# Performance work log

Measured on AMD Instinct MI355X. Metric: run time of the kernel, lower is better.

## Reference

```python
import jax, jax.numpy as jnp
import numpy as np

N, M, K = 500000, 8, 16


def setup_inputs() -> dict:
    key = jax.random.key(0)
    kp, kq, ka, kx = jax.random.split(key, 4)
    p = jax.random.normal(kp, (N, M), dtype=jnp.float32)
    q = jax.random.normal(kq, (N, M), dtype=jnp.float32)
    # scale transitions to be contractive so the length-N recurrence is stable
    a = 0.2 * jax.random.normal(ka, (N, M, M), dtype=jnp.float32)
    x = jax.random.normal(kx, (N, K), dtype=jnp.float32)
    return {"p": p, "q": q, "a": a, "x": x}


def reference(p, q, a, x):
    # StrictLowerTriQSM.matmul: y_i = p_i @ f_i, with recurrence
    # f_{i+1} = a_i @ f_i + outer(q_i, x_i), f_0 = 0.  f has shape (M, K).
    def impl(f, data):
        qi, ai, xi = data
        return ai @ f + jnp.outer(qi, xi), f

    init = jnp.zeros((M, x.shape[1]), dtype=x.dtype)
    _, f = jax.lax.scan(impl, init, (q, a, x))  # f: (N, M, K)
    return jnp.einsum("nm,nmk->nk", p, f)
```

## Files before the change

### kernel.cpp

```cpp
#include <hip/hip_runtime.h>


#define NTOT 500000

#define AS1(p) ((const __attribute__((address_space(1))) void*)(p))
#define AS3(p) ((__attribute__((address_space(3))) void*)(p))
#define GLOAD_LDS16(gp, lp) __builtin_amdgcn_global_load_lds(AS1(gp), AS3(lp), 16, 0, 0)
#define GLOAD_LDS4(gp, lp)  __builtin_amdgcn_global_load_lds(AS1(gp), AS3(lp), 4, 0, 0)
#define WAIT_VM(n) asm volatile("s_waitcnt vmcnt(" #n ")" ::: "memory")

static __device__ __forceinline__ int iminc(int a, int b) { return a < b ? a : b; }

template<int NC> struct P {
  static constexpr int CH   = (NC == 16384) ? 32 : 64;
  static constexpr int NST  = CH / 2;
  static constexpr int NG   = NC / 64;
  static constexpr int NS   = NG / 64;
  static constexpr int AGGA = 0;
  static constexpr int AGGB = NC * 64;
  static constexpr int GAGA = NC * 192;
  static constexpr int GAGB = NC * 192 + NG * 64;
  static constexpr int SGA  = NC * 192 + NG * 192;
  static constexpr int SGB  = NC * 192 + NG * 192 + NS * 64;
  static constexpr size_t BYTES = (size_t)(NC * 192 + NG * 192 + NS * 192) * 4u;
};

#define K1_COMP(E, VBS, VAS, VBD, VAD) do {                                  \
    const float xk_ = xgb[(E) * 16];                                         \
    const float4 q0_ = *(const float4*)(qgb + (E) * 8);                      \
    const float4 q1_ = *(const float4*)(qgb + (E) * 8 + 4);                  \
    const float qv_[8] = {q0_.x,q0_.y,q0_.z,q0_.w,q1_.x,q1_.y,q1_.z,q1_.w};  \
    _Pragma("unroll") for (int mm = 0; mm < 8; ++mm) {                       \
      const float4 r0_ = *(const float4*)(agb + (E) * 256 + mm * 8);         \
      const float4 r1_ = *(const float4*)(agb + (E) * 256 + mm * 8 + 4);     \
      VBD[mm] = qv_[mm] * xk_                                                \
              + r0_.x*VBS[0] + r0_.y*VBS[1] + r0_.z*VBS[2] + r0_.w*VBS[3]    \
              + r1_.x*VBS[4] + r1_.y*VBS[5] + r1_.z*VBS[6] + r1_.w*VBS[7];   \
      VAD[mm] = r0_.x*VAS[0] + r0_.y*VAS[1] + r0_.z*VAS[2] + r0_.w*VAS[3]    \
              + r1_.x*VAS[4] + r1_.y*VAS[5] + r1_.z*VAS[6] + r1_.w*VAS[7];   \
    }                                                                        \
  } while (0)

template<int NC>
__global__ __launch_bounds__(256, 4) void k1_aggregate(
    const float* __restrict__ q, const float* __restrict__ a,
    const float* __restrict__ x, float* __restrict__ ws)
{
  using PP = P<NC>;
  constexpr int CH = PP::CH, NST = PP::NST;
  __shared__ float sm[4 * 3 * 704];
  const int wv   = (int)(threadIdx.x >> 6);
  const int wave = blockIdx.x * 4 + wv;
  const int lane = (int)(threadIdx.x & 63);
  const int g    = lane >> 4;
  const int ll   = lane & 15;
  const int c    = wave * 4 + g;
  const bool hasA = ll >= 8;
  const int acol  = ll & 7;

  const int cb = wave * 4;
  float* b0 = sm + wv * 2112;
  float* b1 = b0 + 704;
  float* b2 = b0 + 1408;

  const int goff = g * 64;
  const int qoff = 512 + g * 16;
  const int xoff = 576 + (g >> 1) * 64 + (g & 1) * 32 + ll;

  float vB0[8], vA0[8], vB1[8], vA1[8];
#pragma unroll
  for (int m = 0; m < 8; ++m) { vB0[m] = 0.f; vA0[m] = 0.f; }
  if (hasA) vA0[acol] = 1.f;

  const int gl = lane >> 4, ql = lane & 15;
  auto stage = [&](int ss, float* lb) {
    const int base = cb * CH + ss * 2;
    GLOAD_LDS16(a + (size_t)iminc(base + gl * CH,     NTOT - 1) * 64u + ql * 4, lb);
    GLOAD_LDS16(a + (size_t)iminc(base + gl * CH + 1, NTOT - 1) * 64u + ql * 4, lb + 256);
    GLOAD_LDS4 (q + (size_t)iminc(base + (lane >> 4) * CH + ((lane >> 3) & 1), NTOT - 1) * 8u  + (lane & 7),  lb + 512);
    GLOAD_LDS4 (x + (size_t)iminc(base + (lane >> 5) * CH + ((lane >> 4) & 1), NTOT - 1) * 16u + (lane & 15), lb + 576);
    GLOAD_LDS4 (x + (size_t)iminc(base + (2 + (lane >> 5)) * CH + ((lane >> 4) & 1), NTOT - 1) * 16u + (lane & 15), lb + 640);
  };

  stage(0, b0);
  stage(1, b1);
#pragma unroll 1
  for (int ss = 0; ss < NST; ++ss) {
    float* lb = b0;
    if (ss + 2 < NST) {
      stage(ss + 2, b2);
      WAIT_VM(10);
    } else if (ss + 1 < NST) {
      WAIT_VM(5);
    } else {
      WAIT_VM(0);
    }
    const float* agb = lb + goff;
    const float* qgb = lb + qoff;
    const float* xgb = lb + xoff;
    K1_COMP(0, vB0, vA0, vB1, vA1);
    K1_COMP(1, vB1, vA1, vB0, vA0);
    float* t = b0; b0 = b1; b1 = b2; b2 = t;
  }

  {
    float* dst = ws + PP::AGGB + (size_t)c * 128u + (size_t)ll * 8u;
#pragma unroll
    for (int m = 0; m < 8; ++m) dst[m] = vB0[m];
  }
  if (hasA) {
    float* dst = ws + PP::AGGA + (size_t)c * 64u + (size_t)acol * 8u;
#pragma unroll
    for (int m = 0; m < 8; ++m) dst[m] = vA0[m];
  }
}

template<int NC, int LV>
__global__ __launch_bounds__(64) void k2scan(float* __restrict__ ws)
{
  using PP = P<NC>;
  constexpr int OFFAIN  = (LV == 0) ? PP::AGGA : PP::GAGA;
  constexpr int OFFBIN  = (LV == 0) ? PP::AGGB : PP::GAGB;
  constexpr int OFFAOUT = (LV == 0) ? PP::GAGA : PP::SGA;
  constexpr int OFFBOUT = (LV == 0) ? PP::GAGB : PP::SGB;
  __shared__ float sA[64 * 64];
  const int g    = blockIdx.x;
  const int lane = (int)(threadIdx.x & 63);
  const bool isB = lane < 16;
  const bool isA = (lane >= 16) && (lane < 24);
  const int bcol = lane & 15;
  const int acol = (lane - 16) & 7;

#pragma unroll 1
  for (int t = 0; t < 16; ++t)
    GLOAD_LDS16(ws + OFFAIN + (size_t)g * 4096u + t * 256 + lane * 4, sA + t * 256);

  float v[8];
#pragma unroll
  for (int m = 0; m < 8; ++m) v[m] = 0.f;
  if (isA) v[acol] = 1.f;

  float4 nb0, nb1;
  {
    const float* s = ws + OFFBIN + (size_t)(g * 64) * 128u + (size_t)bcol * 8u;
    nb0 = *(const float4*)s; nb1 = *(const float4*)(s + 4);
  }
  WAIT_VM(0);

#pragma unroll 1
  for (int j = 0; j < 64; ++j) {
    const int c = g * 64 + j;
    float bB[8] = {nb0.x, nb0.y, nb0.z, nb0.w, nb1.x, nb1.y, nb1.z, nb1.w};
    if (j + 1 < 64) {
      const float* s = ws + OFFBIN + (size_t)(c + 1) * 128u + (size_t)bcol * 8u;
      nb0 = *(const float4*)s; nb1 = *(const float4*)(s + 4);
    }
    if (isB) {
      float* dst = ws + OFFBIN + (size_t)c * 128u + (size_t)bcol * 8u;
#pragma unroll
      for (int m = 0; m < 8; ++m) dst[m] = v[m];
    } else if (isA) {
      float* dst = ws + OFFAIN + (size_t)c * 64u + (size_t)acol * 8u;
#pragma unroll
      for (int m = 0; m < 8; ++m) dst[m] = v[m];
    }
    const float* Aj = sA + j * 64;
    float nv[8];
#pragma unroll
    for (int m = 0; m < 8; ++m) nv[m] = 0.f;
#pragma unroll
    for (int t = 0; t < 8; ++t) {
      float4 col0 = *(const float4*)(Aj + t * 8);
      float4 col1 = *(const float4*)(Aj + t * 8 + 4);
      nv[0] += col0.x * v[t]; nv[1] += col0.y * v[t];
      nv[2] += col0.z * v[t]; nv[3] += col0.w * v[t];
      nv[4] += col1.x * v[t]; nv[5] += col1.y * v[t];
      nv[6] += col1.z * v[t]; nv[7] += col1.w * v[t];
    }
    if (isB) {
#pragma unroll
      for (int m = 0; m < 8; ++m) nv[m] += bB[m];
    }
#pragma unroll
    for (int m = 0; m < 8; ++m) v[m] = nv[m];
  }

  if (isB) {
    float* dst = ws + OFFBOUT + (size_t)g * 128u + (size_t)bcol * 8u;
#pragma unroll
    for (int m = 0; m < 8; ++m) dst[m] = v[m];
  } else if (isA) {
    float* dst = ws + OFFAOUT + (size_t)g * 64u + (size_t)acol * 8u;
#pragma unroll
    for (int m = 0; m < 8; ++m) dst[m] = v[m];
  }
}

template<int NC>
__global__ __launch_bounds__(64) void k2c_topscan(float* __restrict__ ws)
{
  using PP = P<NC>;
  const int lane = (int)(threadIdx.x & 63);
  const bool isB = lane < 16;
  const int bcol = lane & 15;

  float v[8];
#pragma unroll
  for (int m = 0; m < 8; ++m) v[m] = 0.f;

#pragma unroll 1
  for (int j = 0; j < PP::NS; ++j) {
    float bB[8];
    if (isB) {
      const float* s = ws + PP::SGB + (size_t)j * 128u + (size_t)bcol * 8u;
#pragma unroll
      for (int m = 0; m < 8; ++m) bB[m] = s[m];
      float* dst = ws + PP::SGB + (size_t)j * 128u + (size_t)bcol * 8u;
#pragma unroll
      for (int m = 0; m < 8; ++m) dst[m] = v[m];
    }
    const float* Aj = ws + PP::SGA + (size_t)j * 64u;
    float nv[8];
#pragma unroll
    for (int m = 0; m < 8; ++m) nv[m] = 0.f;
#pragma unroll
    for (int t = 0; t < 8; ++t) {
      float4 col0 = *(const float4*)(Aj + t * 8);
      float4 col1 = *(const float4*)(Aj + t * 8 + 4);
      nv[0] += col0.x * v[t]; nv[1] += col0.y * v[t];
      nv[2] += col0.z * v[t]; nv[3] += col0.w * v[t];
      nv[4] += col1.x * v[t]; nv[5] += col1.y * v[t];
      nv[6] += col1.z * v[t]; nv[7] += col1.w * v[t];
    }
    if (isB) {
#pragma unroll
      for (int m = 0; m < 8; ++m) nv[m] += bB[m];
    }
#pragma unroll
    for (int m = 0; m < 8; ++m) v[m] = nv[m];
  }
}

#define K3_COMP(E, FS, FD) do {                                              \
    const float xk_ = xgb[(E) * 16];                                         \
    const float4 q0_ = *(const float4*)(qgb + (E) * 8);                      \
    const float4 q1_ = *(const float4*)(qgb + (E) * 8 + 4);                  \
    const float4 p0_ = *(const float4*)(pgb + (E) * 8);                      \
    const float4 p1_ = *(const float4*)(pgb + (E) * 8 + 4);                  \
    const float y_ = p0_.x*FS[0] + p0_.y*FS[1] + p0_.z*FS[2] + p0_.w*FS[3]   \
                   + p1_.x*FS[4] + p1_.y*FS[5] + p1_.z*FS[6] + p1_.w*FS[7];  \
    const int i_ = c * CH + ss * 2 + (E);                                    \
    if (i_ < NTOT) out[(size_t)i_ * 16u + k] = y_;                           \
    const float qv_[8] = {q0_.x,q0_.y,q0_.z,q0_.w,q1_.x,q1_.y,q1_.z,q1_.w};  \
    _Pragma("unroll") for (int mm = 0; mm < 8; ++mm) {                       \
      const float4 r0_ = *(const float4*)(agb + (E) * 256 + mm * 8);         \
      const float4 r1_ = *(const float4*)(agb + (E) * 256 + mm * 8 + 4);     \
      FD[mm] = qv_[mm] * xk_                                                 \
             + r0_.x*FS[0] + r0_.y*FS[1] + r0_.z*FS[2] + r0_.w*FS[3]         \
             + r1_.x*FS[4] + r1_.y*FS[5] + r1_.z*FS[6] + r1_.w*FS[7];        \
    }                                                                        \
  } while (0)

template<int NC>
__global__ __launch_bounds__(256, 4) void k3_output(
    const float* __restrict__ p, const float* __restrict__ q,
    const float* __restrict__ a, const float* __restrict__ x,
    const float* __restrict__ ws, float* __restrict__ out)
{
  using PP = P<NC>;
  constexpr int CH = PP::CH, NST = PP::NST;
  __shared__ float sm3[4 * 3 * 768];
  const int wv   = (int)(threadIdx.x >> 6);
  const int wave = blockIdx.x * 4 + wv;
  const int lane = (int)(threadIdx.x & 63);
  const int g    = lane >> 4;
  const int k    = lane & 15;
  const int c    = wave * 4 + g;
  const int gr   = c >> 6;
  const int sidx = gr >> 6;

  const int cb = wave * 4;
  float* b0 = sm3 + wv * 2304;
  float* b1 = b0 + 768;
  float* b2 = b0 + 1536;

  const int goff = g * 64;
  const int qoff = 512 + g * 16;
  const int poff = 576 + g * 16;
  const int xoff = 640 + (g >> 1) * 64 + (g & 1) * 32 + k;

  auto stage = [&](int ss, float* lb) {
    const int base = cb * CH + ss * 2;
    GLOAD_LDS16(a + (size_t)iminc(base + (lane >> 4) * CH,     NTOT - 1) * 64u + (lane & 15) * 4, lb);
    GLOAD_LDS16(a + (size_t)iminc(base + (lane >> 4) * CH + 1, NTOT - 1) * 64u + (lane & 15) * 4, lb + 256);
    GLOAD_LDS4 (q + (size_t)iminc(base + (lane >> 4) * CH + ((lane >> 3) & 1), NTOT - 1) * 8u  + (lane & 7),  lb + 512);
    GLOAD_LDS4 (p + (size_t)iminc(base + (lane >> 4) * CH + ((lane >> 3) & 1), NTOT - 1) * 8u  + (lane & 7),  lb + 576);
    GLOAD_LDS4 (x + (size_t)iminc(base + (lane >> 5) * CH + ((lane >> 4) & 1), NTOT - 1) * 16u + (lane & 15), lb + 640);
    GLOAD_LDS4 (x + (size_t)iminc(base + (2 + (lane >> 5)) * CH + ((lane >> 4) & 1), NTOT - 1) * 16u + (lane & 15), lb + 704);
  };

  stage(0, b0);
  stage(1, b1);

  const float* __restrict__ sBc = ws + PP::SGB  + (size_t)sidx * 128u + (size_t)k * 8u;
  const float* __restrict__ gBc = ws + PP::GAGB + (size_t)gr   * 128u + (size_t)k * 8u;
  const float* __restrict__ gA  = ws + PP::GAGA + (size_t)gr   * 64u;
  const float* __restrict__ pA  = ws + PP::AGGA + (size_t)c    * 64u;
  const float* __restrict__ lBc = ws + PP::AGGB + (size_t)c    * 128u + (size_t)k * 8u;
  float t1[8];
#pragma unroll
  for (int m = 0; m < 8; ++m) t1[m] = gBc[m];
#pragma unroll
  for (int t = 0; t < 8; ++t) {
    float4 c0 = *(const float4*)(gA + t * 8);
    float4 c1 = *(const float4*)(gA + t * 8 + 4);
    const float st = sBc[t];
    t1[0] += c0.x * st; t1[1] += c0.y * st; t1[2] += c0.z * st; t1[3] += c0.w * st;
    t1[4] += c1.x * st; t1[5] += c1.y * st; t1[6] += c1.z * st; t1[7] += c1.w * st;
  }
  float f0[8], f1[8];
#pragma unroll
  for (int m = 0; m < 8; ++m) f0[m] = lBc[m];
#pragma unroll
  for (int t = 0; t < 8; ++t) {
    float4 c0 = *(const float4*)(pA + t * 8);
    float4 c1 = *(const float4*)(pA + t * 8 + 4);
    const float gt = t1[t];
    f0[0] += c0.x * gt; f0[1] += c0.y * gt; f0[2] += c0.z * gt; f0[3] += c0.w * gt;
    f0[4] += c1.x * gt; f0[5] += c1.y * gt; f0[6] += c1.z * gt; f0[7] += c1.w * gt;
  }

#pragma unroll 1
  for (int ss = 0; ss < NST; ++ss) {
    float* lb = b0;
    if (ss + 2 < NST) {
      stage(ss + 2, b2);
      WAIT_VM(12);
    } else if (ss + 1 < NST) {
      WAIT_VM(6);
    } else {
      WAIT_VM(0);
    }
    const float* agb = lb + goff;
    const float* qgb = lb + qoff;
    const float* pgb = lb + poff;
    const float* xgb = lb + xoff;
    K3_COMP(0, f0, f1);
    K3_COMP(1, f1, f0);
    float* t = b0; b0 = b1; b1 = b2; b2 = t;
  }
}

template<int NC>
static void launch_all(const float* p, const float* q, const float* a,
                       const float* x, float* out, float* ws, hipStream_t stream)
{
  using PP = P<NC>;
  hipLaunchKernelGGL(HIP_KERNEL_NAME(k1_aggregate<NC>), dim3(NC / 16), dim3(256), 0, stream, q, a, x, ws);
  hipLaunchKernelGGL(HIP_KERNEL_NAME(k2scan<NC, 0>),    dim3(PP::NG),  dim3(64),  0, stream, ws);
  hipLaunchKernelGGL(HIP_KERNEL_NAME(k2scan<NC, 1>),    dim3(PP::NS),  dim3(64),  0, stream, ws);
  hipLaunchKernelGGL(HIP_KERNEL_NAME(k2c_topscan<NC>),  dim3(1),       dim3(64),  0, stream, ws);
  hipLaunchKernelGGL(HIP_KERNEL_NAME(k3_output<NC>),    dim3(NC / 16), dim3(256), 0, stream, p, q, a, x, ws, out);
}

extern "C" void kernel_launch(void* const* d_in, const int* in_sizes, int n_in,
                              void* d_out, int out_size, void* d_ws, size_t ws_size,
                              hipStream_t stream)
{
  const float* p = (const float*)d_in[0];
  const float* q = (const float*)d_in[1];
  const float* a = (const float*)d_in[2];
  const float* x = (const float*)d_in[3];
  float* out = (float*)d_out;
  float* ws  = (float*)d_ws;

  if (ws_size >= P<16384>::BYTES) {
    launch_all<16384>(p, q, a, x, out, ws, stream);
  } else {
    launch_all<8192>(p, q, a, x, out, ws, stream);
  }
}
```

Baseline: 157.8 us.

## Add 32768-chunk configuration and switch staging to double-buffered LDS

New measurement: 162.2 us. 2.8% more time.

```diff
diff --git a/kernel.cpp b/kernel.cpp
--- a/kernel.cpp
+++ b/kernel.cpp
@@ -12,7 +12,7 @@
 static __device__ __forceinline__ int iminc(int a, int b) { return a < b ? a : b; }
 
 template<int NC> struct P {
-  static constexpr int CH   = (NC == 16384) ? 32 : 64;
+  static constexpr int CH   = 524288 / NC;
   static constexpr int NST  = CH / 2;
   static constexpr int NG   = NC / 64;
   static constexpr int NS   = NG / 64;
@@ -48,7 +48,7 @@
 {
   using PP = P<NC>;
   constexpr int CH = PP::CH, NST = PP::NST;
-  __shared__ float sm[4 * 3 * 704];
+  __shared__ float sm[4 * 2 * 704];
   const int wv   = (int)(threadIdx.x >> 6);
   const int wave = blockIdx.x * 4 + wv;
   const int lane = (int)(threadIdx.x & 63);
@@ -59,9 +59,8 @@
   const int acol  = ll & 7;
 
   const int cb = wave * 4;
-  float* b0 = sm + wv * 2112;
+  float* b0 = sm + wv * 1408;
   float* b1 = b0 + 704;
-  float* b2 = b0 + 1408;
 
   const int goff = g * 64;
   const int qoff = 512 + g * 16;
@@ -83,24 +82,17 @@
   };
 
   stage(0, b0);
-  stage(1, b1);
 #pragma unroll 1
   for (int ss = 0; ss < NST; ++ss) {
-    float* lb = b0;
-    if (ss + 2 < NST) {
-      stage(ss + 2, b2);
-      WAIT_VM(10);
-    } else if (ss + 1 < NST) {
-      WAIT_VM(5);
-    } else {
-      WAIT_VM(0);
-    }
-    const float* agb = lb + goff;
-    const float* qgb = lb + qoff;
-    const float* xgb = lb + xoff;
+    float* cur = (ss & 1) ? b1 : b0;
+    float* nxt = (ss & 1) ? b0 : b1;
+    if (ss + 1 < NST) { stage(ss + 1, nxt); WAIT_VM(5); }
+    else              { WAIT_VM(0); }
+    const float* agb = cur + goff;
+    const float* qgb = cur + qoff;
+    const float* xgb = cur + xoff;
     K1_COMP(0, vB0, vA0, vB1, vA1);
     K1_COMP(1, vB1, vA1, vB0, vA0);
-    float* t = b0; b0 = b1; b1 = b2; b2 = t;
   }
 
   {
@@ -269,7 +261,7 @@
 {
   using PP = P<NC>;
   constexpr int CH = PP::CH, NST = PP::NST;
-  __shared__ float sm3[4 * 3 * 768];
+  __shared__ float sm3[4 * 2 * 768];
   const int wv   = (int)(threadIdx.x >> 6);
   const int wave = blockIdx.x * 4 + wv;
   const int lane = (int)(threadIdx.x & 63);
@@ -280,9 +272,8 @@
   const int sidx = gr >> 6;
 
   const int cb = wave * 4;
-  float* b0 = sm3 + wv * 2304;
+  float* b0 = sm3 + wv * 1536;
   float* b1 = b0 + 768;
-  float* b2 = b0 + 1536;
 
   const int goff = g * 64;
   const int qoff = 512 + g * 16;
@@ -299,9 +290,6 @@
     GLOAD_LDS4 (x + (size_t)iminc(base + (2 + (lane >> 5)) * CH + ((lane >> 4) & 1), NTOT - 1) * 16u + (lane & 15), lb + 704);
   };
 
-  stage(0, b0);
-  stage(1, b1);
-
   const float* __restrict__ sBc = ws + PP::SGB  + (size_t)sidx * 128u + (size_t)k * 8u;
   const float* __restrict__ gBc = ws + PP::GAGB + (size_t)gr   * 128u + (size_t)k * 8u;
   const float* __restrict__ gA  = ws + PP::GAGA + (size_t)gr   * 64u;
@@ -329,25 +317,21 @@
     f0[0] += c0.x * gt; f0[1] += c0.y * gt; f0[2] += c0.z * gt; f0[3] += c0.w * gt;
     f0[4] += c1.x * gt; f0[5] += c1.y * gt; f0[6] += c1.z * gt; f0[7] += c1.w * gt;
   }
-
+  asm volatile("" ::: "memory");
+
+  stage(0, b0);
 #pragma unroll 1
   for (int ss = 0; ss < NST; ++ss) {
-    float* lb = b0;
-    if (ss + 2 < NST) {
-      stage(ss + 2, b2);
-      WAIT_VM(12);
-    } else if (ss + 1 < NST) {
-      WAIT_VM(6);
-    } else {
-      WAIT_VM(0);
-    }
-    const float* agb = lb + goff;
-    const float* qgb = lb + qoff;
-    const float* pgb = lb + poff;
-    const float* xgb = lb + xoff;
+    float* cur = (ss & 1) ? b1 : b0;
+    float* nxt = (ss & 1) ? b0 : b1;
+    if (ss + 1 < NST) { stage(ss + 1, nxt); WAIT_VM(6); }
+    else              { WAIT_VM(0); }
+    const float* agb = cur + goff;
+    const float* qgb = cur + qoff;
+    const float* pgb = cur + poff;
+    const float* xgb = cur + xoff;
     K3_COMP(0, f0, f1);
     K3_COMP(1, f1, f0);
-    float* t = b0; b0 = b1; b1 = b2; b2 = t;
   }
 }
 
@@ -374,7 +358,9 @@
   float* out = (float*)d_out;
   float* ws  = (float*)d_ws;
 
-  if (ws_size >= P<16384>::BYTES) {
+  if (ws_size >= P<32768>::BYTES) {
+    launch_all<32768>(p, q, a, x, out, ws, stream);
+  } else if (ws_size >= P<16384>::BYTES) {
     launch_all<16384>(p, q, a, x, out, ws, stream);
   } else {
     launch_all<8192>(p, q, a, x, out, ws, stream);
```
